# Optimization experiments

Measured on AMD Instinct MI355X. Metric: run time of the kernel, lower is better.

Reference implementation:

```python
import jax, jax.numpy as jnp
import numpy as np

N, E, D, L, G = 50000, 200000, 200, 10, 2500
FEAT = 200
EPS = 1e-5  # BatchNorm1d eps
SELF_LOOP_BOND_TYPE = 4


def _xavier(key, shape):
    fan_in, fan_out = shape[-2], shape[-1]
    lim = float(np.sqrt(6.0 / (fan_in + fan_out)))
    return jax.random.uniform(key, shape, jnp.float32, -lim, lim)


def setup_inputs() -> dict:
    key = jax.random.key(0)
    ks = jax.random.split(key, 16)
    x = jax.random.randint(ks[0], (N, 2), 0, 3)
    edge_index = jax.random.randint(ks[1], (2, E), 0, N)
    edge_attr = jax.random.randint(ks[2], (E, 2), 0, 3)
    batch = jnp.sort(jax.random.randint(ks[3], (N,), 0, G))
    return dict(
        x=x, edge_index=edge_index, edge_attr=edge_attr, batch=batch,
        x_emb1=_xavier(ks[4], (500, D)),
        x_emb2=_xavier(ks[5], (500, D)),
        edge_emb1_w=_xavier(ks[6], (L, 5, D)),
        edge_emb2_w=_xavier(ks[7], (L, 3, D)),
        mlp_w1=_xavier(ks[8], (L, D, 2 * D)), mlp_b1=jnp.zeros((L, 2 * D), jnp.float32),
        mlp_w2=_xavier(ks[9], (L, 2 * D, D)), mlp_b2=jnp.zeros((L, D), jnp.float32),
        bn_gamma=jnp.ones((L, D), jnp.float32), bn_beta=jnp.zeros((L, D), jnp.float32),
        feat_w=_xavier(ks[10], (D, FEAT)), feat_b=jnp.zeros((FEAT,), jnp.float32),
        out_w1=_xavier(ks[11], (FEAT, FEAT)), out_b1=jnp.zeros((FEAT,), jnp.float32),
        out_w2=_xavier(ks[12], (FEAT, FEAT // 2)), out_b2=jnp.zeros((FEAT // 2,), jnp.float32),
    )


def reference(x, edge_index, edge_attr, batch,
              x_emb1, x_emb2, edge_emb1_w, edge_emb2_w,
              mlp_w1, mlp_b1, mlp_w2, mlp_b2, bn_gamma, bn_beta,
              feat_w, feat_b, out_w1, out_b1, out_w2, out_b2):
    src, dst = edge_index[0], edge_index[1]
    h = x_emb1[x[:, 0]] + x_emb2[x[:, 1]]  # [N, D]
    n = h.shape[0]
    for l in range(L):
        # edge embeddings for real edges; self-loops get attr (4, 0)
        e_emb = edge_emb1_w[l][edge_attr[:, 0]] + edge_emb2_w[l][edge_attr[:, 1]]  # [E, D]
        self_emb = edge_emb1_w[l][SELF_LOOP_BOND_TYPE] + edge_emb2_w[l][0]          # [D]
        msg = h[src] + e_emb                                                        # [E, D]
        aggr = jax.ops.segment_sum(msg, dst, num_segments=n) + h + self_emb         # add-aggr incl. self loops
        # GINE update MLP: D -> 2D -> D
        h1 = jax.nn.relu(aggr @ mlp_w1[l] + mlp_b1[l])
        h = h1 @ mlp_w2[l] + mlp_b2[l]
        # BatchNorm1d (training-mode batch stats, biased var)
        mu = h.mean(axis=0)
        var = jnp.mean((h - mu) ** 2, axis=0)
        h = (h - mu) * jax.lax.rsqrt(var + EPS) * bn_gamma[l] + bn_beta[l]
        if l < L - 1:  # last layer: dropout only (p=0 -> identity), no relu
            h = jax.nn.relu(h)
    # global mean pool over graphs
    counts = jnp.maximum(jax.ops.segment_sum(jnp.ones((n,), h.dtype), batch, num_segments=G), 1.0)
    h_global = jax.ops.segment_sum(h, batch, num_segments=G) / counts[:, None]  # [G, D]
    h_global = h_global @ feat_w + feat_b
    out = jax.nn.relu(h_global @ out_w1 + out_b1) @ out_w2 + out_b2  # [G, FEAT//2]
    # out_global and out_sub are computed identically in the source
    return (h_global, out, out)
```

## Files before the change

kernel.cpp:

```cpp
#include <hip/hip_runtime.h>

#define N_NODES 50000
#define N_EDGES 200000
#define D 200
#define NLAYERS 10
#define NGRAPH 2500
#define EPS 1e-5f

typedef unsigned short u16;
typedef unsigned int u32;
typedef __attribute__((ext_vector_type(8))) __bf16 bf16x8;
typedef __attribute__((ext_vector_type(4))) float f32x4;

__device__ __forceinline__ u16 f2bf_rne(float x) {
    union { float f; unsigned u; } c; c.f = x;
    unsigned r = c.u + 0x7FFF + ((c.u >> 16) & 1);
    return (u16)(r >> 16);
}
__device__ __forceinline__ u32 split_pack(float x) {
    u16 h = f2bf_rne(x);
    union { unsigned u; float f; } c; c.u = ((unsigned)h) << 16;
    u16 l = f2bf_rne(x - c.f);
    return (u32)h | ((u32)l << 16);
}


__global__ void count_kernel(const int* __restrict__ dst, int* __restrict__ counts) {
    int e = blockIdx.x * 256 + threadIdx.x;
    if (e < N_EDGES) atomicAdd(&counts[dst[e]], 1);
}

__global__ void scan1_kernel(const int* __restrict__ counts, int* __restrict__ psum) {
    __shared__ int s[256];
    int idx = blockIdx.x * 256 + threadIdx.x;
    s[threadIdx.x] = (idx < N_NODES) ? counts[idx] : 0;
    __syncthreads();
    for (int off = 128; off > 0; off >>= 1) {
        if (threadIdx.x < off) s[threadIdx.x] += s[threadIdx.x + off];
        __syncthreads();
    }
    if (threadIdx.x == 0) psum[blockIdx.x] = s[0];
}

__global__ void scan2_kernel(const int* __restrict__ psum, int* __restrict__ poff, int nchunk) {
    __shared__ int s[256];
    int t = threadIdx.x;
    int v = (t < nchunk) ? psum[t] : 0;
    s[t] = v;
    __syncthreads();
    for (int off = 1; off < 256; off <<= 1) {
        int xv = (t >= off) ? s[t - off] : 0;
        __syncthreads();
        s[t] += xv;
        __syncthreads();
    }
    if (t < nchunk) poff[t] = s[t] - v;
}

__global__ void scan3_kernel(const int* __restrict__ counts, const int* __restrict__ poff,
                             int* __restrict__ row_start, int* __restrict__ cursor) {
    __shared__ int s[256];
    int t = threadIdx.x;
    int idx = blockIdx.x * 256 + t;
    int v = (idx < N_NODES) ? counts[idx] : 0;
    s[t] = v;
    __syncthreads();
    for (int off = 1; off < 256; off <<= 1) {
        int xv = (t >= off) ? s[t - off] : 0;
        __syncthreads();
        s[t] += xv;
        __syncthreads();
    }
    if (idx < N_NODES) {
        int rs = poff[blockIdx.x] + s[t] - v;
        row_start[idx] = rs;
        cursor[idx] = rs;
    }
    if (blockIdx.x == 0 && t == 0) row_start[N_NODES] = N_EDGES;
}

__global__ void scatter_kernel(const int* __restrict__ dst, int* __restrict__ cursor,
                               int* __restrict__ edge_list) {
    int e = blockIdx.x * 256 + threadIdx.x;
    if (e < N_EDGES) {
        int p = atomicAdd(&cursor[dst[e]], 1);
        edge_list[p] = e;
    }
}

__global__ void bounds_kernel(const int* __restrict__ batch, int* __restrict__ gstart) {
    int g = blockIdx.x * 256 + threadIdx.x;
    if (g > NGRAPH) return;
    if (g == NGRAPH) { gstart[NGRAPH] = N_NODES; return; }
    int lo = 0, hi = N_NODES;
    while (lo < hi) { int mid = (lo + hi) >> 1; if (batch[mid] < g) lo = mid + 1; else hi = mid; }
    gstart[g] = lo;
}


__global__ void prep_w1_kernel(const float* __restrict__ w, u32* __restrict__ wp) {
    int idx = blockIdx.x * 256 + threadIdx.x;
    if (idx >= NLAYERS * 512 * 224) return;
    int k = idx % 224;
    int n = (idx / 224) % 512;
    int l = idx / (224 * 512);
    float v = (k < 200 && n < 400) ? w[((size_t)l * 200 + k) * 400 + n] : 0.f;
    wp[idx] = split_pack(v);
}

__global__ void prep_w2_kernel(const float* __restrict__ w, u32* __restrict__ wp) {
    int idx = blockIdx.x * 256 + threadIdx.x;
    if (idx >= NLAYERS * 256 * 416) return;
    int k = idx % 416;
    int n = (idx / 416) % 256;
    int l = idx / (416 * 256);
    float v = (k < 400 && n < 200) ? w[((size_t)l * 400 + k) * 200 + n] : 0.f;
    wp[idx] = split_pack(v);
}


__global__ void embed_kernel(const int* __restrict__ x, const float* __restrict__ emb1,
                             const float* __restrict__ emb2, float* __restrict__ h) {
    int idx = blockIdx.x * 256 + threadIdx.x;
    if (idx >= N_NODES * 50) return;
    int node = idx / 50;
    int c = (idx % 50) * 4;
    int a = x[node * 2], b = x[node * 2 + 1];
    float4 v1 = *(const float4*)(emb1 + (size_t)a * D + c);
    float4 v2 = *(const float4*)(emb2 + (size_t)b * D + c);
    float4 o;
    o.x = v1.x + v2.x; o.y = v1.y + v2.y; o.z = v1.z + v2.z; o.w = v1.w + v2.w;
    *(float4*)(h + (size_t)node * D + c) = o;
}


template <int HAS_BN>
__global__ void aggregate_kernel(const float* __restrict__ hin,
                                 const float* __restrict__ stats,
                                 const float* __restrict__ gamma, const float* __restrict__ beta,
                                 const float* __restrict__ e1, const float* __restrict__ e2,
                                 const int* __restrict__ row_start, const int* __restrict__ edge_list,
                                 const int* __restrict__ src, const int* __restrict__ edge_attr,
                                 u32* __restrict__ Ap) {
    __shared__ float t1[5 * D];
    __shared__ float t2[3 * D];
    for (int i = threadIdx.x; i < 5 * D; i += 256) t1[i] = e1[i];
    for (int i = threadIdx.x; i < 3 * D; i += 256) t2[i] = e2[i];
    __syncthreads();
    int idx = blockIdx.x * 256 + threadIdx.x;
    if (idx >= N_NODES * 56) return;
    int node = idx / 56;
    int c = (idx % 56) * 4;
    size_t ob = (size_t)node * 224 + c;
    if (c >= 200) {
        *(uint4*)(Ap + ob) = make_uint4(0u, 0u, 0u, 0u);
        return;
    }
    float a[4], b[4];
    if (HAS_BN) {
        const float invN = 1.0f / (float)N_NODES;
#pragma unroll
        for (int j = 0; j < 4; ++j) {
            float s = stats[c + j], q = stats[256 + c + j];
            float m = s * invN;
            float var = q * invN - m * m;
            float sc = gamma[c + j] * rsqrtf(var + EPS);
            a[j] = sc; b[j] = beta[c + j] - m * sc;
        }
    }
    float4 acc = *(const float4*)(hin + (size_t)node * D + c);
    if (HAS_BN) {
        acc.x = fmaxf(acc.x * a[0] + b[0], 0.f);
        acc.y = fmaxf(acc.y * a[1] + b[1], 0.f);
        acc.z = fmaxf(acc.z * a[2] + b[2], 0.f);
        acc.w = fmaxf(acc.w * a[3] + b[3], 0.f);
    }
    acc.x += t1[4 * D + c + 0] + t2[c + 0];
    acc.y += t1[4 * D + c + 1] + t2[c + 1];
    acc.z += t1[4 * D + c + 2] + t2[c + 2];
    acc.w += t1[4 * D + c + 3] + t2[c + 3];
    int jb = row_start[node], je = row_start[node + 1];
    for (int j = jb; j < je; ++j) {
        int e = edge_list[j];
        int s = src[e];
        int2 eav = *(const int2*)(edge_attr + 2 * e);
        float4 hv = *(const float4*)(hin + (size_t)s * D + c);
        if (HAS_BN) {
            hv.x = fmaxf(hv.x * a[0] + b[0], 0.f);
            hv.y = fmaxf(hv.y * a[1] + b[1], 0.f);
            hv.z = fmaxf(hv.z * a[2] + b[2], 0.f);
            hv.w = fmaxf(hv.w * a[3] + b[3], 0.f);
        }
        const float* p1 = t1 + eav.x * D + c;
        const float* p2 = t2 + eav.y * D + c;
        acc.x += hv.x + p1[0] + p2[0];
        acc.y += hv.y + p1[1] + p2[1];
        acc.z += hv.z + p1[2] + p2[2];
        acc.w += hv.w + p1[3] + p2[3];
    }
    uint4 pv;
    pv.x = split_pack(acc.x); pv.y = split_pack(acc.y);
    pv.z = split_pack(acc.z); pv.w = split_pack(acc.w);
    *(uint4*)(Ap + ob) = pv;
}


template <int FM, int FN, int RELU, int WRITE_PACKED, int STATS>
__global__ __launch_bounds__(256) void gemm_mfma(
    const u32* __restrict__ Ap, const u32* __restrict__ Bp,
    const float* __restrict__ bias,
    float* __restrict__ Cf, u32* __restrict__ Cp,
    float* __restrict__ stats,
    int M, int Kpad, int Nc, int NcPad, int KT)
{
    constexpr int BMT = FM * 32;
    constexpr int BNTL = FN * 32;
    constexpr int RA = BMT / 64;
    constexpr int RB = BNTL / 64;

    __shared__ alignas(16) u16 sAh[BMT * 32];
    __shared__ alignas(16) u16 sAl[BMT * 32];
    __shared__ alignas(16) u16 sBh[BNTL * 32];
    __shared__ alignas(16) u16 sBl[BNTL * 32];

    const int tid = threadIdx.x;
    const int lane = tid & 63;
    const int wid = tid >> 6;
    const int wm = wid >> 1, wn = wid & 1;
    const int lr = lane & 15, lg = lane >> 4;
    const int bm0 = blockIdx.y * BMT;
    const int bn0 = blockIdx.x * BNTL;

    const int r0 = tid >> 2;
    const int gd = tid & 3;
    const int slot = gd ^ ((r0 >> 1) & 3);
    const int lO0 = r0 * 32 + slot * 8;
    const size_t gA = (size_t)(bm0 + r0) * Kpad + gd * 8;
    const size_t gB = (size_t)(bn0 + r0) * Kpad + gd * 8;

    f32x4 acc[FM][FN];
#pragma unroll
    for (int i = 0; i < FM; ++i)
#pragma unroll
        for (int j = 0; j < FN; ++j) acc[i][j] = (f32x4){0.f, 0.f, 0.f, 0.f};

    int aoff[FM], boff[FN];
#pragma unroll
    for (int f = 0; f < FM; ++f) {
        int arow = wm * FM * 16 + f * 16 + lr;
        aoff[f] = arow * 32 + ((lg ^ ((arow >> 1) & 3)) * 8);
    }
#pragma unroll
    for (int f = 0; f < FN; ++f) {
        int brow = wn * FN * 16 + f * 16 + lr;
        boff[f] = brow * 32 + ((lg ^ ((brow >> 1) & 3)) * 8);
    }

    uint4 pa[RA][2], pb[RB][2];
#define LOADT(K0)                                                                        \
    {                                                                                    \
        _Pragma("unroll")                                                                \
        for (int rr = 0; rr < RA; ++rr) {                                                \
            pa[rr][0] = *(const uint4*)(Ap + gA + (size_t)rr * 64 * Kpad + (K0));        \
            pa[rr][1] = *(const uint4*)(Ap + gA + (size_t)rr * 64 * Kpad + (K0) + 4);    \
        }                                                                                \
        _Pragma("unroll")                                                                \
        for (int rr = 0; rr < RB; ++rr) {                                                \
            pb[rr][0] = *(const uint4*)(Bp + gB + (size_t)rr * 64 * Kpad + (K0));        \
            pb[rr][1] = *(const uint4*)(Bp + gB + (size_t)rr * 64 * Kpad + (K0) + 4);    \
        }                                                                                \
    }

#define UNPACK_STORE(a, b, ph, pl)                                        \
    {                                                                     \
        uint4 hh, ll;                                                     \
        hh.x = __byte_perm((a).x, (a).y, 0x5410);                         \
        hh.y = __byte_perm((a).z, (a).w, 0x5410);                         \
        hh.z = __byte_perm((b).x, (b).y, 0x5410);                         \
        hh.w = __byte_perm((b).z, (b).w, 0x5410);                         \
        ll.x = __byte_perm((a).x, (a).y, 0x7632);                         \
        ll.y = __byte_perm((a).z, (a).w, 0x7632);                         \
        ll.z = __byte_perm((b).x, (b).y, 0x7632);                         \
        ll.w = __byte_perm((b).z, (b).w, 0x7632);                         \
        *(uint4*)(ph) = hh;                                               \
        *(uint4*)(pl) = ll;                                               \
    }

    LOADT(0)
    for (int kt = 0; kt < KT; ++kt) {
        if (kt > 0) __syncthreads();
#pragma unroll
        for (int rr = 0; rr < RA; ++rr)
            UNPACK_STORE(pa[rr][0], pa[rr][1], sAh + rr * 2048 + lO0, sAl + rr * 2048 + lO0)
#pragma unroll
        for (int rr = 0; rr < RB; ++rr)
            UNPACK_STORE(pb[rr][0], pb[rr][1], sBh + rr * 2048 + lO0, sBl + rr * 2048 + lO0)
        __syncthreads();
        if (kt + 1 < KT) { LOADT((size_t)(kt + 1) * 32) }

        bf16x8 fbh[FN], fbl[FN];
#pragma unroll
        for (int fn = 0; fn < FN; ++fn) {
            fbh[fn] = *(const bf16x8*)(sBh + boff[fn]);
            fbl[fn] = *(const bf16x8*)(sBl + boff[fn]);
        }
#pragma unroll
        for (int fm = 0; fm < FM; ++fm) {
            bf16x8 fah = *(const bf16x8*)(sAh + aoff[fm]);
            bf16x8 fal = *(const bf16x8*)(sAl + aoff[fm]);
#pragma unroll
            for (int fn = 0; fn < FN; ++fn) {
                acc[fm][fn] = __builtin_amdgcn_mfma_f32_16x16x32_bf16(fah, fbh[fn], acc[fm][fn], 0, 0, 0);
                acc[fm][fn] = __builtin_amdgcn_mfma_f32_16x16x32_bf16(fah, fbl[fn], acc[fm][fn], 0, 0, 0);
                acc[fm][fn] = __builtin_amdgcn_mfma_f32_16x16x32_bf16(fal, fbh[fn], acc[fm][fn], 0, 0, 0);
            }
        }
    }
#undef LOADT
#undef UNPACK_STORE

#pragma unroll
    for (int fn = 0; fn < FN; ++fn) {
        int col = bn0 + wn * FN * 16 + fn * 16 + lr;
        float bv = (col < Nc) ? bias[col] : 0.f;
        if (WRITE_PACKED) {
            if (col < NcPad) {
#pragma unroll
                for (int fm = 0; fm < FM; ++fm) {
#pragma unroll
                    for (int r = 0; r < 4; ++r) {
                        int row = bm0 + wm * FM * 16 + fm * 16 + lg * 4 + r;
                        if (row < M) {
                            float v = acc[fm][fn][r] + bv;
                            if (RELU) v = fmaxf(v, 0.f);
                            if (col >= Nc) v = 0.f;
                            Cp[(size_t)row * NcPad + col] = split_pack(v);
                        }
                    }
                }
            }
        } else {
            float s = 0.f, q = 0.f;
#pragma unroll
            for (int fm = 0; fm < FM; ++fm) {
#pragma unroll
                for (int r = 0; r < 4; ++r) {
                    int row = bm0 + wm * FM * 16 + fm * 16 + lg * 4 + r;
                    if (row < M && col < Nc) {
                        float v = acc[fm][fn][r] + bv;
                        if (RELU) v = fmaxf(v, 0.f);
                        Cf[(size_t)row * Nc + col] = v;
                        if (STATS) { s += v; q += v * v; }
                    }
                }
            }
            if (STATS) {
                s += __shfl_xor(s, 16); s += __shfl_xor(s, 32);
                q += __shfl_xor(q, 16); q += __shfl_xor(q, 32);
                if (lg == 0 && col < Nc) {
                    atomicAdd(&stats[col], s);
                    atomicAdd(&stats[256 + col], q);
                }
            }
        }
    }
}


#define BM 128
#define BNT 64
#define BK 8

__global__ __launch_bounds__(256) void gemm_kernel(const float* __restrict__ A,
                                                   const float* __restrict__ W,
                                                   const float* __restrict__ bias,
                                                   float* __restrict__ C,
                                                   int M, int K, int Nc, int relu) {
    __shared__ float As[BK][BM];
    __shared__ float Bs[BK][BNT];
    int tid = threadIdx.x;
    int bm = blockIdx.x * BM;
    int bn = blockIdx.y * BNT;
    int tx = tid & 15, ty = tid >> 4;

    float acc[8][4];
#pragma unroll
    for (int i = 0; i < 8; ++i)
#pragma unroll
        for (int j = 0; j < 4; ++j) acc[i][j] = 0.f;

    int ar = tid >> 1;
    int ak = (tid & 1) << 2;
    int bk = tid >> 5;
    int bcol = (tid & 31) << 1;

    for (int k0 = 0; k0 < K; k0 += BK) {
        float4 av = {0.f, 0.f, 0.f, 0.f};
        int row = bm + ar;
        if (row < M) av = *(const float4*)(A + (size_t)row * K + k0 + ak);
        As[ak + 0][ar] = av.x; As[ak + 1][ar] = av.y;
        As[ak + 2][ar] = av.z; As[ak + 3][ar] = av.w;
        float2 bv = {0.f, 0.f};
        int col = bn + bcol;
        if (col < Nc) bv = *(const float2*)(W + (size_t)(k0 + bk) * Nc + col);
        Bs[bk][bcol] = bv.x; Bs[bk][bcol + 1] = bv.y;
        __syncthreads();
#pragma unroll
        for (int kk = 0; kk < BK; ++kk) {
            float a[8], b[4];
            *(float4*)(a)     = *(const float4*)(&As[kk][ty * 8]);
            *(float4*)(a + 4) = *(const float4*)(&As[kk][ty * 8 + 4]);
            *(float4*)(b)     = *(const float4*)(&Bs[kk][tx * 4]);
#pragma unroll
            for (int i = 0; i < 8; ++i)
#pragma unroll
                for (int j = 0; j < 4; ++j) acc[i][j] = fmaf(a[i], b[j], acc[i][j]);
        }
        __syncthreads();
    }

#pragma unroll
    for (int i = 0; i < 8; ++i) {
        int row = bm + ty * 8 + i;
        if (row < M) {
            int col = bn + tx * 4;
            if (col < Nc) {
                float4 bb = *(const float4*)(bias + col);
                float4 v;
                v.x = acc[i][0] + bb.x; v.y = acc[i][1] + bb.y;
                v.z = acc[i][2] + bb.z; v.w = acc[i][3] + bb.w;
                if (relu) {
                    v.x = fmaxf(v.x, 0.f); v.y = fmaxf(v.y, 0.f);
                    v.z = fmaxf(v.z, 0.f); v.w = fmaxf(v.w, 0.f);
                }
                *(float4*)(C + (size_t)row * Nc + col) = v;
            }
        }
    }
}


__global__ void pool_bn_kernel(const float* __restrict__ g2, const float* __restrict__ stats,
                               const float* __restrict__ gamma, const float* __restrict__ beta,
                               const int* __restrict__ gstart, float* __restrict__ hg) {
    int idx = blockIdx.x * 256 + threadIdx.x;
    if (idx >= NGRAPH * 50) return;
    int g = idx / 50;
    int c = (idx % 50) * 4;
    float a[4], b[4];
    const float invN = 1.0f / (float)N_NODES;
#pragma unroll
    for (int j = 0; j < 4; ++j) {
        float s = stats[c + j], q = stats[256 + c + j];
        float m = s * invN;
        float var = q * invN - m * m;
        float sc = gamma[c + j] * rsqrtf(var + EPS);
        a[j] = sc; b[j] = beta[c + j] - m * sc;
    }
    int s0 = gstart[g], e0 = gstart[g + 1];
    float4 acc = {0.f, 0.f, 0.f, 0.f};
    for (int r = s0; r < e0; ++r) {
        float4 v = *(const float4*)(g2 + (size_t)r * D + c);
        acc.x += v.x; acc.y += v.y; acc.z += v.z; acc.w += v.w;
    }
    float inv = 1.0f / fmaxf((float)(e0 - s0), 1.0f);
    acc.x = acc.x * inv * a[0] + b[0];
    acc.y = acc.y * inv * a[1] + b[1];
    acc.z = acc.z * inv * a[2] + b[2];
    acc.w = acc.w * inv * a[3] + b[3];
    *(float4*)(hg + (size_t)g * D + c) = acc;
}


extern "C" void kernel_launch(void* const* d_in, const int* in_sizes, int n_in,
                              void* d_out, int out_size, void* d_ws, size_t ws_size,
                              hipStream_t stream) {
    const int*   x       = (const int*)d_in[0];
    const int*   ei      = (const int*)d_in[1];
    const int*   ea      = (const int*)d_in[2];
    const int*   batch   = (const int*)d_in[3];
    const float* x_emb1  = (const float*)d_in[4];
    const float* x_emb2  = (const float*)d_in[5];
    const float* e1w     = (const float*)d_in[6];
    const float* e2w     = (const float*)d_in[7];
    const float* w1      = (const float*)d_in[8];
    const float* b1      = (const float*)d_in[9];
    const float* w2      = (const float*)d_in[10];
    const float* b2      = (const float*)d_in[11];
    const float* gamma   = (const float*)d_in[12];
    const float* beta    = (const float*)d_in[13];
    const float* feat_w  = (const float*)d_in[14];
    const float* feat_b  = (const float*)d_in[15];
    const float* out_w1  = (const float*)d_in[16];
    const float* out_b1  = (const float*)d_in[17];
    const float* out_w2  = (const float*)d_in[18];
    const float* out_b2  = (const float*)d_in[19];
    const int* src = ei;
    const int* dst = ei + N_EDGES;

    char* p = (char*)d_ws;
    auto alloc = [&](size_t bytes) -> void* {
        void* r = (void*)p;
        p += (bytes + 255) & ~(size_t)255;
        return r;
    };
    const int MPAD = 50048;
    float* h      = (float*)alloc((size_t)N_NODES * D * 4);
    float* g2     = h;
    u32*   aggrP  = (u32*)alloc((size_t)MPAD * 224 * 4);
    u32*   h1p    = (u32*)alloc((size_t)MPAD * 416 * 4);
    u32*   wt1p   = (u32*)alloc((size_t)NLAYERS * 512 * 224 * 4);
    u32*   wt2p   = (u32*)alloc((size_t)NLAYERS * 256 * 416 * 4);
    int*   counts    = (int*)alloc(N_NODES * 4);
    int*   row_start = (int*)alloc((N_NODES + 1) * 4);
    int*   cursor    = (int*)alloc(N_NODES * 4);
    int*   edge_list = (int*)alloc(N_EDGES * 4);
    int*   psum      = (int*)alloc(256 * 4);
    int*   poff      = (int*)alloc(256 * 4);
    int*   gstart    = (int*)alloc((NGRAPH + 1) * 4);
    float* stats     = (float*)alloc(512 * 4);
    float* hg        = (float*)alloc((size_t)NGRAPH * D * 4);
    float* tbuf      = (float*)alloc((size_t)NGRAPH * D * 4);
    float* outf      = (float*)d_out;

    const int NCHUNK = (N_NODES + 255) / 256;

    prep_w1_kernel<<<(NLAYERS * 512 * 224 + 255) / 256, 256, 0, stream>>>(w1, wt1p);
    prep_w2_kernel<<<(NLAYERS * 256 * 416 + 255) / 256, 256, 0, stream>>>(w2, wt2p);

    hipMemsetAsync(counts, 0, N_NODES * 4, stream);
    count_kernel<<<(N_EDGES + 255) / 256, 256, 0, stream>>>(dst, counts);
    scan1_kernel<<<NCHUNK, 256, 0, stream>>>(counts, psum);
    scan2_kernel<<<1, 256, 0, stream>>>(psum, poff, NCHUNK);
    scan3_kernel<<<NCHUNK, 256, 0, stream>>>(counts, poff, row_start, cursor);
    scatter_kernel<<<(N_EDGES + 255) / 256, 256, 0, stream>>>(dst, cursor, edge_list);
    bounds_kernel<<<(NGRAPH + 1 + 255) / 256, 256, 0, stream>>>(batch, gstart);

    embed_kernel<<<(N_NODES * 50 + 255) / 256, 256, 0, stream>>>(x, x_emb1, x_emb2, h);

    dim3 g1(4, 391);
    dim3 g2d(2, 782);
    for (int l = 0; l < NLAYERS; ++l) {
        if (l == 0)
            aggregate_kernel<0><<<(N_NODES * 56 + 255) / 256, 256, 0, stream>>>(
                h, nullptr, nullptr, nullptr,
                e1w, e2w, row_start, edge_list, src, ea, aggrP);
        else
            aggregate_kernel<1><<<(N_NODES * 56 + 255) / 256, 256, 0, stream>>>(
                g2, stats, gamma + (size_t)(l - 1) * D, beta + (size_t)(l - 1) * D,
                e1w + (size_t)l * 5 * D, e2w + (size_t)l * 3 * D,
                row_start, edge_list, src, ea, aggrP);
        gemm_mfma<4, 4, 1, 1, 0><<<g1, 256, 0, stream>>>(
            aggrP, wt1p + (size_t)l * 512 * 224,
            b1 + (size_t)l * 400, nullptr, h1p, nullptr, N_NODES, 224, 400, 416, 7);
        hipMemsetAsync(stats, 0, 512 * 4, stream);
        gemm_mfma<2, 4, 0, 0, 1><<<g2d, 256, 0, stream>>>(
            h1p, wt2p + (size_t)l * 256 * 416,
            b2 + (size_t)l * 200, g2, nullptr, stats, N_NODES, 416, 200, 200, 13);
    }

    pool_bn_kernel<<<(NGRAPH * 50 + 255) / 256, 256, 0, stream>>>(
        g2, stats, gamma + (size_t)(NLAYERS - 1) * D, beta + (size_t)(NLAYERS - 1) * D,
        gstart, hg);

    dim3 gp((NGRAPH + BM - 1) / BM, (D + BNT - 1) / BNT);
    gemm_kernel<<<gp, 256, 0, stream>>>(hg, feat_w, feat_b, outf, NGRAPH, D, D, 0);
    gemm_kernel<<<gp, 256, 0, stream>>>(outf, out_w1, out_b1, tbuf, NGRAPH, D, D, 1);
    dim3 go((NGRAPH + BM - 1) / BM, (100 + BNT - 1) / BNT);
    gemm_kernel<<<go, 256, 0, stream>>>(tbuf, out_w2, out_b2, outf + (size_t)NGRAPH * D,
                                        NGRAPH, D, 100, 0);
    hipMemcpyAsync(outf + (size_t)NGRAPH * D + (size_t)NGRAPH * 100,
                   outf + (size_t)NGRAPH * D,
                   (size_t)NGRAPH * 100 * 4, hipMemcpyDeviceToDevice, stream);
}
```

Before: 2.245 ms.

## Load GEMM tiles directly to LDS and remap blocks across XCDs

```diff
diff --git a/kernel.cpp b/kernel.cpp
--- a/kernel.cpp
+++ b/kernel.cpp
@@ -12,6 +12,13 @@
 typedef __attribute__((ext_vector_type(8))) __bf16 bf16x8;
 typedef __attribute__((ext_vector_type(4))) float f32x4;
 
+typedef __attribute__((address_space(3))) u32 as3_u32;
+typedef __attribute__((address_space(1))) const u32 as1_u32;
+
+__device__ __forceinline__ void gload16(const u32* g, u32* l) {
+    __builtin_amdgcn_global_load_lds((as1_u32*)g, (as3_u32*)l, 16, 0, 0);
+}
+
 __device__ __forceinline__ u16 f2bf_rne(float x) {
     union { float f; unsigned u; } c; c.f = x;
     unsigned r = c.u + 0x7FFF + ((c.u >> 16) & 1);
@@ -22,6 +29,15 @@
     union { unsigned u; float f; } c; c.u = ((unsigned)h) << 16;
     u16 l = f2bf_rne(x - c.f);
     return (u32)h | ((u32)l << 16);
+}
+
+__device__ __forceinline__ void unpack_pair(uint4 q1, uint4 q2, bf16x8& hi, bf16x8& lo) {
+    uint4 h, l;
+    h.x = __byte_perm(q1.x, q1.y, 0x5410); h.y = __byte_perm(q1.z, q1.w, 0x5410);
+    h.z = __byte_perm(q2.x, q2.y, 0x5410); h.w = __byte_perm(q2.z, q2.w, 0x5410);
+    l.x = __byte_perm(q1.x, q1.y, 0x7632); l.y = __byte_perm(q1.z, q1.w, 0x7632);
+    l.z = __byte_perm(q2.x, q2.y, 0x7632); l.w = __byte_perm(q2.z, q2.w, 0x7632);
+    hi = *(bf16x8*)&h; lo = *(bf16x8*)&l;
 }
 
 
@@ -205,7 +221,7 @@
 }
 
 
-template <int FM, int FN, int RELU, int WRITE_PACKED, int STATS>
+template <int FM, int FN, int GXL, int RELU, int WRITE_PACKED, int STATS>
 __global__ __launch_bounds__(256) void gemm_mfma(
     const u32* __restrict__ Ap, const u32* __restrict__ Bp,
     const float* __restrict__ bias,
@@ -215,28 +231,44 @@
 {
     constexpr int BMT = FM * 32;
     constexpr int BNTL = FN * 32;
-    constexpr int RA = BMT / 64;
-    constexpr int RB = BNTL / 64;
-
-    __shared__ alignas(16) u16 sAh[BMT * 32];
-    __shared__ alignas(16) u16 sAl[BMT * 32];
-    __shared__ alignas(16) u16 sBh[BNTL * 32];
-    __shared__ alignas(16) u16 sBl[BNTL * 32];
+    constexpr int NIA = BMT / 32;
+    constexpr int NIB = BNTL / 32;
+
+    __shared__ alignas(16) u32 sA[BMT * 32];
+    __shared__ alignas(16) u32 sB[BNTL * 32];
 
     const int tid = threadIdx.x;
     const int lane = tid & 63;
-    const int wid = tid >> 6;
-    const int wm = wid >> 1, wn = wid & 1;
+    const int w = tid >> 6;
+    const int wm = w >> 1, wn = w & 1;
     const int lr = lane & 15, lg = lane >> 4;
-    const int bm0 = blockIdx.y * BMT;
-    const int bn0 = blockIdx.x * BNTL;
-
-    const int r0 = tid >> 2;
-    const int gd = tid & 3;
-    const int slot = gd ^ ((r0 >> 1) & 3);
-    const int lO0 = r0 * 32 + slot * 8;
-    const size_t gA = (size_t)(bm0 + r0) * Kpad + gd * 8;
-    const size_t gB = (size_t)(bn0 + r0) * Kpad + gd * 8;
+
+    const int nwg = (int)(gridDim.x * gridDim.y);
+    const int id = (int)(blockIdx.y * gridDim.x + blockIdx.x);
+    const int q = nwg >> 3, rm = nwg & 7;
+    const int xcd = id & 7, sub = id >> 3;
+    const int wgid = (xcd < rm ? xcd * (q + 1) : rm * (q + 1) + (xcd - rm) * q) + sub;
+    const int bm0 = (wgid >> GXL) * BMT;
+    const int bn0 = (wgid & ((1 << GXL) - 1)) * BNTL;
+
+    const u32* ga[NIA]; const u32* gb[NIB];
+    u32* la[NIA]; u32* lb[NIB];
+#pragma unroll
+    for (int i = 0; i < NIA; ++i) {
+        int c = w * NIA + i;
+        int r = c * 8 + (lane >> 3);
+        int j = (lane & 7) ^ (r & 7);
+        ga[i] = Ap + (size_t)(bm0 + r) * Kpad + j * 4;
+        la[i] = sA + c * 256;
+    }
+#pragma unroll
+    for (int i = 0; i < NIB; ++i) {
+        int c = w * NIB + i;
+        int r = c * 8 + (lane >> 3);
+        int j = (lane & 7) ^ (r & 7);
+        gb[i] = Bp + (size_t)(bn0 + r) * Kpad + j * 4;
+        lb[i] = sB + c * 256;
+    }
 
     f32x4 acc[FM][FN];
 #pragma unroll
@@ -244,70 +276,36 @@
 #pragma unroll
         for (int j = 0; j < FN; ++j) acc[i][j] = (f32x4){0.f, 0.f, 0.f, 0.f};
 
+    const int sx = lr & 7;
+    const int u1 = ((2 * lg) ^ sx) * 4;
+    const int u2 = ((2 * lg + 1) ^ sx) * 4;
     int aoff[FM], boff[FN];
 #pragma unroll
-    for (int f = 0; f < FM; ++f) {
-        int arow = wm * FM * 16 + f * 16 + lr;
-        aoff[f] = arow * 32 + ((lg ^ ((arow >> 1) & 3)) * 8);
-    }
-#pragma unroll
-    for (int f = 0; f < FN; ++f) {
-        int brow = wn * FN * 16 + f * 16 + lr;
-        boff[f] = brow * 32 + ((lg ^ ((brow >> 1) & 3)) * 8);
-    }
-
-    uint4 pa[RA][2], pb[RB][2];
-#define LOADT(K0)                                                                        \
-    {                                                                                    \
-        _Pragma("unroll")                                                                \
-        for (int rr = 0; rr < RA; ++rr) {                                                \
-            pa[rr][0] = *(const uint4*)(Ap + gA + (size_t)rr * 64 * Kpad + (K0));        \
-            pa[rr][1] = *(const uint4*)(Ap + gA + (size_t)rr * 64 * Kpad + (K0) + 4);    \
-        }                                                                                \
-        _Pragma("unroll")                                                                \
-        for (int rr = 0; rr < RB; ++rr) {                                                \
-            pb[rr][0] = *(const uint4*)(Bp + gB + (size_t)rr * 64 * Kpad + (K0));        \
-            pb[rr][1] = *(const uint4*)(Bp + gB + (size_t)rr * 64 * Kpad + (K0) + 4);    \
-        }                                                                                \
-    }
-
-#define UNPACK_STORE(a, b, ph, pl)                                        \
-    {                                                                     \
-        uint4 hh, ll;                                                     \
-        hh.x = __byte_perm((a).x, (a).y, 0x5410);                         \
-        hh.y = __byte_perm((a).z, (a).w, 0x5410);                         \
-        hh.z = __byte_perm((b).x, (b).y, 0x5410);                         \
-        hh.w = __byte_perm((b).z, (b).w, 0x5410);                         \
-        ll.x = __byte_perm((a).x, (a).y, 0x7632);                         \
-        ll.y = __byte_perm((a).z, (a).w, 0x7632);                         \
-        ll.z = __byte_perm((b).x, (b).y, 0x7632);                         \
-        ll.w = __byte_perm((b).z, (b).w, 0x7632);                         \
-        *(uint4*)(ph) = hh;                                               \
-        *(uint4*)(pl) = ll;                                               \
-    }
-
-    LOADT(0)
+    for (int f = 0; f < FM; ++f) aoff[f] = (wm * FM * 16 + f * 16 + lr) * 32;
+#pragma unroll
+    for (int f = 0; f < FN; ++f) boff[f] = (wn * FN * 16 + f * 16 + lr) * 32;
+
     for (int kt = 0; kt < KT; ++kt) {
-        if (kt > 0) __syncthreads();
-#pragma unroll
-        for (int rr = 0; rr < RA; ++rr)
-            UNPACK_STORE(pa[rr][0], pa[rr][1], sAh + rr * 2048 + lO0, sAl + rr * 2048 + lO0)
-#pragma unroll
-        for (int rr = 0; rr < RB; ++rr)
-            UNPACK_STORE(pb[rr][0], pb[rr][1], sBh + rr * 2048 + lO0, sBl + rr * 2048 + lO0)
-        __syncthreads();
-        if (kt + 1 < KT) { LOADT((size_t)(kt + 1) * 32) }
+        const int ko = kt * 32;
+#pragma unroll
+        for (int i = 0; i < NIA; ++i) gload16(ga[i] + ko, la[i]);
+#pragma unroll
+        for (int i = 0; i < NIB; ++i) gload16(gb[i] + ko, lb[i]);
+        __syncthreads();
 
         bf16x8 fbh[FN], fbl[FN];
 #pragma unroll
         for (int fn = 0; fn < FN; ++fn) {
-            fbh[fn] = *(const bf16x8*)(sBh + boff[fn]);
-            fbl[fn] = *(const bf16x8*)(sBl + boff[fn]);
+            uint4 q1 = *(const uint4*)(sB + boff[fn] + u1);
+            uint4 q2 = *(const uint4*)(sB + boff[fn] + u2);
+            unpack_pair(q1, q2, fbh[fn], fbl[fn]);
         }
 #pragma unroll
         for (int fm = 0; fm < FM; ++fm) {
-            bf16x8 fah = *(const bf16x8*)(sAh + aoff[fm]);
-            bf16x8 fal = *(const bf16x8*)(sAl + aoff[fm]);
+            uint4 q1 = *(const uint4*)(sA + aoff[fm] + u1);
+            uint4 q2 = *(const uint4*)(sA + aoff[fm] + u2);
+            bf16x8 fah, fal;
+            unpack_pair(q1, q2, fah, fal);
 #pragma unroll
             for (int fn = 0; fn < FN; ++fn) {
                 acc[fm][fn] = __builtin_amdgcn_mfma_f32_16x16x32_bf16(fah, fbh[fn], acc[fm][fn], 0, 0, 0);
@@ -315,9 +313,8 @@
                 acc[fm][fn] = __builtin_amdgcn_mfma_f32_16x16x32_bf16(fal, fbh[fn], acc[fm][fn], 0, 0, 0);
             }
         }
-    }
-#undef LOADT
-#undef UNPACK_STORE
+        __syncthreads();
+    }
 
 #pragma unroll
     for (int fn = 0; fn < FN; ++fn) {
@@ -340,7 +337,7 @@
                 }
             }
         } else {
-            float s = 0.f, q = 0.f;
+            float s = 0.f, q2 = 0.f;
 #pragma unroll
             for (int fm = 0; fm < FM; ++fm) {
 #pragma unroll
@@ -350,16 +347,16 @@
                         float v = acc[fm][fn][r] + bv;
                         if (RELU) v = fmaxf(v, 0.f);
                         Cf[(size_t)row * Nc + col] = v;
-                        if (STATS) { s += v; q += v * v; }
+                        if (STATS) { s += v; q2 += v * v; }
                     }
                 }
             }
             if (STATS) {
                 s += __shfl_xor(s, 16); s += __shfl_xor(s, 32);
-                q += __shfl_xor(q, 16); q += __shfl_xor(q, 32);
+                q2 += __shfl_xor(q2, 16); q2 += __shfl_xor(q2, 32);
                 if (lg == 0 && col < Nc) {
                     atomicAdd(&stats[col], s);
-                    atomicAdd(&stats[256 + col], q);
+                    atomicAdd(&stats[256 + col], q2);
                 }
             }
         }
@@ -550,11 +547,11 @@
                 g2, stats, gamma + (size_t)(l - 1) * D, beta + (size_t)(l - 1) * D,
                 e1w + (size_t)l * 5 * D, e2w + (size_t)l * 3 * D,
                 row_start, edge_list, src, ea, aggrP);
-        gemm_mfma<4, 4, 1, 1, 0><<<g1, 256, 0, stream>>>(
+        gemm_mfma<4, 4, 2, 1, 1, 0><<<g1, 256, 0, stream>>>(
             aggrP, wt1p + (size_t)l * 512 * 224,
             b1 + (size_t)l * 400, nullptr, h1p, nullptr, N_NODES, 224, 400, 416, 7);
         hipMemsetAsync(stats, 0, 512 * 4, stream);
-        gemm_mfma<2, 4, 0, 0, 1><<<g2d, 256, 0, stream>>>(
+        gemm_mfma<2, 4, 1, 0, 0, 1><<<g2d, 256, 0, stream>>>(
             h1p, wt2p + (size_t)l * 256 * 416,
             b2 + (size_t)l * 200, g2, nullptr, stats, N_NODES, 416, 200, 200, 13);
     }
```

After: 2.405 ms. +7.1%, slower.

## Remap GEMM workgroups per XCD, enlarge second GEMM tile, one node per wave

Applied to the files above, without the earlier changes.

```diff
diff --git a/kernel.cpp b/kernel.cpp
--- a/kernel.cpp
+++ b/kernel.cpp
@@ -147,10 +147,10 @@
     for (int i = threadIdx.x; i < 5 * D; i += 256) t1[i] = e1[i];
     for (int i = threadIdx.x; i < 3 * D; i += 256) t2[i] = e2[i];
     __syncthreads();
-    int idx = blockIdx.x * 256 + threadIdx.x;
-    if (idx >= N_NODES * 56) return;
-    int node = idx / 56;
-    int c = (idx % 56) * 4;
+    int node = blockIdx.x * 4 + (threadIdx.x >> 6);
+    int lane = threadIdx.x & 63;
+    if (node >= N_NODES || lane >= 56) return;
+    int c = lane * 4;
     size_t ob = (size_t)node * 224 + c;
     if (c >= 200) {
         *(uint4*)(Ap + ob) = make_uint4(0u, 0u, 0u, 0u);
@@ -205,7 +205,7 @@
 }
 
 
-template <int FM, int FN, int RELU, int WRITE_PACKED, int STATS>
+template <int FM, int FN, int GXL, int RELU, int WRITE_PACKED, int STATS>
 __global__ __launch_bounds__(256) void gemm_mfma(
     const u32* __restrict__ Ap, const u32* __restrict__ Bp,
     const float* __restrict__ bias,
@@ -228,8 +228,14 @@
     const int wid = tid >> 6;
     const int wm = wid >> 1, wn = wid & 1;
     const int lr = lane & 15, lg = lane >> 4;
-    const int bm0 = blockIdx.y * BMT;
-    const int bn0 = blockIdx.x * BNTL;
+
+    const int nwg = (int)(gridDim.x * gridDim.y);
+    const int id = (int)(blockIdx.y * gridDim.x + blockIdx.x);
+    const int q = nwg >> 3, rm = nwg & 7;
+    const int xcd = id & 7, sub = id >> 3;
+    const int wgid = (xcd < rm ? xcd * (q + 1) : rm * (q + 1) + (xcd - rm) * q) + sub;
+    const int bm0 = (wgid >> GXL) * BMT;
+    const int bn0 = (wgid & ((1 << GXL) - 1)) * BNTL;
 
     const int r0 = tid >> 2;
     const int gd = tid & 3;
@@ -340,7 +346,7 @@
                 }
             }
         } else {
-            float s = 0.f, q = 0.f;
+            float s = 0.f, q2 = 0.f;
 #pragma unroll
             for (int fm = 0; fm < FM; ++fm) {
 #pragma unroll
@@ -350,16 +356,16 @@
                         float v = acc[fm][fn][r] + bv;
                         if (RELU) v = fmaxf(v, 0.f);
                         Cf[(size_t)row * Nc + col] = v;
-                        if (STATS) { s += v; q += v * v; }
+                        if (STATS) { s += v; q2 += v * v; }
                     }
                 }
             }
             if (STATS) {
                 s += __shfl_xor(s, 16); s += __shfl_xor(s, 32);
-                q += __shfl_xor(q, 16); q += __shfl_xor(q, 32);
+                q2 += __shfl_xor(q2, 16); q2 += __shfl_xor(q2, 32);
                 if (lg == 0 && col < Nc) {
                     atomicAdd(&stats[col], s);
-                    atomicAdd(&stats[256 + col], q);
+                    atomicAdd(&stats[256 + col], q2);
                 }
             }
         }
@@ -539,22 +545,22 @@
     embed_kernel<<<(N_NODES * 50 + 255) / 256, 256, 0, stream>>>(x, x_emb1, x_emb2, h);
 
     dim3 g1(4, 391);
-    dim3 g2d(2, 782);
+    dim3 g2d(2, 391);
     for (int l = 0; l < NLAYERS; ++l) {
         if (l == 0)
-            aggregate_kernel<0><<<(N_NODES * 56 + 255) / 256, 256, 0, stream>>>(
+            aggregate_kernel<0><<<12500, 256, 0, stream>>>(
                 h, nullptr, nullptr, nullptr,
                 e1w, e2w, row_start, edge_list, src, ea, aggrP);
         else
-            aggregate_kernel<1><<<(N_NODES * 56 + 255) / 256, 256, 0, stream>>>(
+            aggregate_kernel<1><<<12500, 256, 0, stream>>>(
                 g2, stats, gamma + (size_t)(l - 1) * D, beta + (size_t)(l - 1) * D,
                 e1w + (size_t)l * 5 * D, e2w + (size_t)l * 3 * D,
                 row_start, edge_list, src, ea, aggrP);
-        gemm_mfma<4, 4, 1, 1, 0><<<g1, 256, 0, stream>>>(
+        gemm_mfma<4, 4, 2, 1, 1, 0><<<g1, 256, 0, stream>>>(
             aggrP, wt1p + (size_t)l * 512 * 224,
             b1 + (size_t)l * 400, nullptr, h1p, nullptr, N_NODES, 224, 400, 416, 7);
         hipMemsetAsync(stats, 0, 512 * 4, stream);
-        gemm_mfma<2, 4, 0, 0, 1><<<g2d, 256, 0, stream>>>(
+        gemm_mfma<4, 4, 1, 0, 0, 1><<<g2d, 256, 0, stream>>>(
             h1p, wt2p + (size_t)l * 256 * 416,
             b2 + (size_t)l * 200, g2, nullptr, stats, N_NODES, 416, 200, 200, 13);
     }
```

New measurement: 2.139 ms. 4.7% less time.
